# Kernel optimization log

Hardware: AMD Instinct MI355X
Metric: run time of the kernel (lower is better)

Reference implementation:

```python
import jax, jax.numpy as jnp
import numpy as np

D = 512        # d_model
DFF = 2048     # d_ffn
H = 8          # n_heads
L = 4          # n_blocks
EPS = 1e-5     # nn.LayerNorm default eps
NEG = -1e9


def _layer_norm(x, g, b):
    m = jnp.mean(x, axis=-1, keepdims=True)
    v = jnp.var(x, axis=-1, keepdims=True)
    return (x - m) / jnp.sqrt(v + EPS) * g + b


def setup_inputs() -> dict:
    key = jax.random.key(0)
    ks = jax.random.split(key, 6)
    B, S = 2, 2048
    s = 0.02
    x = jax.random.normal(ks[0], (B, S, D), dtype=jnp.float32)
    Wq = jax.random.normal(ks[1], (L, D, D), dtype=jnp.float32) * s
    Wk = jax.random.normal(ks[2], (L, D, D), dtype=jnp.float32) * s
    Wv = jax.random.normal(ks[3], (L, D, D), dtype=jnp.float32) * s
    W1 = jax.random.normal(ks[4], (L, D, DFF), dtype=jnp.float32) * s
    W2 = jax.random.normal(ks[5], (L, DFF, D), dtype=jnp.float32) * s
    z_d = jnp.zeros((L, D), dtype=jnp.float32)
    o_d = jnp.ones((L, D), dtype=jnp.float32)
    return {
        'x': x,
        'Wq': Wq, 'bq': z_d, 'Wk': Wk, 'bk': z_d, 'Wv': Wv, 'bv': z_d,
        'W1': W1, 'b1': jnp.zeros((L, DFF), dtype=jnp.float32),
        'W2': W2, 'b2': z_d,
        'g1': o_d, 'beta1': z_d, 'g2': o_d, 'beta2': z_d,
    }


def reference(x, Wq, bq, Wk, bk, Wv, bv, W1, b1, W2, b2, g1, beta1, g2, beta2):
    B, S, Dm = x.shape
    dk = Dm // H
    scale = 1.0 / (dk ** 0.5)

    def block(h, p):
        wq, bq_, wk, bk_, wv, bv_, w1, b1_, w2, b2_, g1_, be1, g2_, be2 = p
        # QKV projections, split heads: [B,S,D] -> [B,H,S,dk]
        q = (h @ wq + bq_).reshape(B, S, H, dk).transpose(0, 2, 1, 3)
        k = (h @ wk + bk_).reshape(B, S, H, dk).transpose(0, 2, 1, 3)
        v = (h @ wv + bv_).reshape(B, S, H, dk).transpose(0, 2, 1, 3)
        scores = jnp.einsum('bhqd,bhkd->bhqk', q, k) * scale
        # original quirk: padding=0, scores exactly equal to 0 get masked to -1e9
        scores = jnp.where(scores != 0, scores, NEG)
        probs = jax.nn.softmax(scores, axis=-1)
        attn = jnp.einsum('bhqk,bhkd->bhqd', probs, v)
        attn = attn.transpose(0, 2, 1, 3).reshape(B, S, Dm)
        h = _layer_norm(attn + h, g1_, be1)           # add_and_norm1
        ff = jax.nn.relu(h @ w1 + b1_) @ w2 + b2_     # position-wise FFN
        h = _layer_norm(h + ff, g2_, be2)             # add_and_norm2
        return h, None

    params = (Wq, bq, Wk, bk, Wv, bv, W1, b1, W2, b2, g1, beta1, g2, beta2)
    out, _ = jax.lax.scan(block, x, params)
    return out
```

## Files before the change

### kernel.cpp

```cpp
#include <hip/hip_runtime.h>
#include <stdint.h>
#include <math.h>


typedef __bf16 bf16_t;
typedef bf16_t bf16x8 __attribute__((ext_vector_type(8)));
typedef bf16_t bf16x4v __attribute__((ext_vector_type(4)));
typedef float  f32x4  __attribute__((ext_vector_type(4)));

__device__ __forceinline__ f32x4 mfma16(bf16x8 a, bf16x8 b, f32x4 c) {
    return __builtin_amdgcn_mfma_f32_16x16x32_bf16(a, b, c, 0, 0, 0);
}

__device__ __forceinline__ void cp16(const void* g, const void* l) {
    auto gp = reinterpret_cast<const __attribute__((address_space(1))) char*>(
        reinterpret_cast<uintptr_t>(g));
    auto lp = reinterpret_cast<__attribute__((address_space(3))) char*>(
        static_cast<uint32_t>(reinterpret_cast<uintptr_t>(l)));
    __builtin_amdgcn_global_load_lds((const __attribute__((address_space(1))) void*)gp,
                                     (__attribute__((address_space(3))) void*)lp,
                                     16, 0, 0);
}

__global__ void wconv_kernel(const float* __restrict__ Wq, const float* __restrict__ Wk,
                             const float* __restrict__ Wv, const float* __restrict__ W1,
                             const float* __restrict__ W2,
                             bf16_t* __restrict__ oQKV, bf16_t* __restrict__ oW1,
                             bf16_t* __restrict__ oW2)
{
    const int l = blockIdx.y;
    int t = blockIdx.x;
    const float* in; bf16_t* out; int Kd, Nd, tt;
    if (t < 192) {
        int m = t / 64; tt = t % 64; Kd = 512; Nd = 512;
        in  = (m == 0 ? Wq : m == 1 ? Wk : Wv) + (size_t)l * 512 * 512;
        out = oQKV + (size_t)l * 1536 * 512 + (size_t)m * 512 * 512;
    } else if (t < 448) {
        tt = t - 192; Kd = 512; Nd = 2048;
        in  = W1 + (size_t)l * 512 * 2048;
        out = oW1 + (size_t)l * 2048 * 512;
    } else {
        tt = t - 448; Kd = 2048; Nd = 512;
        in  = W2 + (size_t)l * 2048 * 512;
        out = oW2 + (size_t)l * 512 * 2048;
    }
    const int ntx = Nd >> 6;
    const int bk = (tt / ntx) * 64, bn = (tt % ntx) * 64;
    __shared__ float tile[64][65];
    const int tid = threadIdx.x;
    #pragma unroll
    for (int i = 0; i < 16; ++i) {
        int idx = i * 256 + tid; int r = idx >> 6, c = idx & 63;
        tile[r][c] = in[(size_t)(bk + r) * Nd + bn + c];
    }
    __syncthreads();
    #pragma unroll
    for (int i = 0; i < 4; ++i) {
        int idx = i * 256 + tid; int n = idx >> 4, kc = (idx & 15) * 4;
        bf16x4v o;
        o[0] = (bf16_t)tile[kc + 0][n];
        o[1] = (bf16_t)tile[kc + 1][n];
        o[2] = (bf16_t)tile[kc + 2][n];
        o[3] = (bf16_t)tile[kc + 3][n];
        *(bf16x4v*)&out[(size_t)(bn + n) * Kd + bk + kc] = o;
    }
}

__global__ void f2b_kernel(const float* __restrict__ in, bf16_t* __restrict__ out, int n)
{
    int i = (blockIdx.x * 256 + threadIdx.x) * 8;
    if (i >= n) return;
    float4 a = *(const float4*)(in + i);
    float4 b = *(const float4*)(in + i + 4);
    bf16x8 o;
    o[0] = (bf16_t)a.x; o[1] = (bf16_t)a.y; o[2] = (bf16_t)a.z; o[3] = (bf16_t)a.w;
    o[4] = (bf16_t)b.x; o[5] = (bf16_t)b.y; o[6] = (bf16_t)b.z; o[7] = (bf16_t)b.w;
    *(bf16x8*)(out + i) = o;
}

template<int MODE, bool RELU>
__global__ __launch_bounds__(256, 4) void gemm_kernel(
    const bf16_t* __restrict__ A, const bf16_t* __restrict__ Wt,
    const float* __restrict__ b0, const float* __restrict__ b1, const float* __restrict__ b2,
    void* __restrict__ o0, void* __restrict__ o1, void* __restrict__ o2,
    int N, int lda, int klen)
{
    __shared__ __align__(16) bf16_t lA[2][128 * 32];
    __shared__ __align__(16) bf16_t lB[2][128 * 32];
    const int tid = threadIdx.x;
    const int lane = tid & 63, w = tid >> 6;
    const int wm = w >> 1, wn = w & 1;
    const int l15 = lane & 15, quad = lane >> 4;
    const int row0 = blockIdx.y * 128, col0 = blockIdx.x * 128;
    const int kst = blockIdx.z * klen, kend = kst + klen;
    const int wbase = (tid & 192) * 16;

    f32x4 acc[4][4] = {};
    const char* Ab = (const char*)A;
    const char* Bb = (const char*)Wt;

    auto stage = [&](int k0, int buf) {
        #pragma unroll
        for (int p = 0; p < 2; ++p) {
            int o = (p * 256 + tid) * 16;
            int r = o >> 6, cb = o & 63;
            cp16(Ab + ((size_t)(row0 + r) * lda + k0) * 2 + cb, (char*)lA[buf] + p * 4096 + wbase);
            cp16(Bb + ((size_t)(col0 + r) * lda + k0) * 2 + cb, (char*)lB[buf] + p * 4096 + wbase);
        }
    };

    stage(kst, 0);
    int it = 0;
    for (int k0 = kst; k0 < kend; k0 += 32, ++it) {
        __syncthreads();
        if (k0 + 32 < kend) stage(k0 + 32, (it + 1) & 1);
        const bf16_t* cA = lA[it & 1];
        const bf16_t* cB = lB[it & 1];
        bf16x8 af[4], bv_[4];
        #pragma unroll
        for (int i = 0; i < 4; ++i)
            af[i] = *(const bf16x8*)&cA[(wm * 64 + i * 16 + l15) * 32 + quad * 8];
        #pragma unroll
        for (int i = 0; i < 4; ++i)
            bv_[i] = *(const bf16x8*)&cB[(wn * 64 + i * 16 + l15) * 32 + quad * 8];
        #pragma unroll
        for (int mi = 0; mi < 4; ++mi)
            #pragma unroll
            for (int ni = 0; ni < 4; ++ni)
                acc[mi][ni] = mfma16(af[mi], bv_[ni], acc[mi][ni]);
    }

    #pragma unroll
    for (int mi = 0; mi < 4; ++mi) {
        const int rowb = row0 + wm * 64 + mi * 16 + quad * 4;
        #pragma unroll
        for (int ni = 0; ni < 4; ++ni) {
            const int col = col0 + wn * 64 + ni * 16 + l15;
            if (MODE == 1) {
                const float bias = b0[col];
                #pragma unroll
                for (int r = 0; r < 4; ++r) {
                    float v = acc[mi][ni][r] + bias;
                    if (RELU) v = fmaxf(v, 0.f);
                    ((bf16_t*)o0)[(size_t)(rowb + r) * N + col] = (bf16_t)v;
                }
            } else if (MODE == 3) {
                bf16_t* op = (bf16_t*)o0 + (size_t)blockIdx.z * 4096 * 512;
                #pragma unroll
                for (int r = 0; r < 4; ++r)
                    op[(size_t)(rowb + r) * N + col] = (bf16_t)acc[mi][ni][r];
            } else {
                if (col < 512) {
                    const float bias = b0[col];
                    #pragma unroll
                    for (int r = 0; r < 4; ++r)
                        ((bf16_t*)o0)[(size_t)(rowb + r) * 512 + col] =
                            (bf16_t)((acc[mi][ni][r] + bias) * 0.18033688f);
                } else if (col < 1024) {
                    const int c = col - 512;
                    const float bias = b1[c];
                    #pragma unroll
                    for (int r = 0; r < 4; ++r)
                        ((bf16_t*)o1)[(size_t)(rowb + r) * 512 + c] =
                            (bf16_t)(acc[mi][ni][r] + bias);
                } else {
                    const int cv = col - 1024;
                    const int hh = cv >> 6, d = cv & 63;
                    const float bias = b2[cv];
                    const int b_ = rowb >> 11, s = rowb & 2047;
                    bf16x4v pk;
                    #pragma unroll
                    for (int r = 0; r < 4; ++r)
                        pk[r] = (bf16_t)(acc[mi][ni][r] + bias);
                    *(bf16x4v*)&((bf16_t*)o2)[(size_t)((b_ * 8 + hh) * 64 + d) * 2048 + s] = pk;
                }
            }
        }
    }
}

__global__ __launch_bounds__(256, 4) void attn_kernel(
    const bf16_t* __restrict__ Q, const bf16_t* __restrict__ Kg,
    const bf16_t* __restrict__ Vt, bf16_t* __restrict__ Op,
    float* __restrict__ Lb)
{
    __shared__ __align__(16) bf16_t lK[2][64 * 32];
    __shared__ __align__(16) bf16_t lV[2][64 * 32];
    __shared__ __align__(16) bf16_t lP[4][1152];
    const int tid = threadIdx.x;
    const int lane = tid & 63, w = tid >> 6;
    const int l15 = lane & 15, quad = lane >> 4;
    const int bh = blockIdx.x & 15, sp = blockIdx.x >> 4;
    const int b = bh >> 3, h = bh & 7;
    const int q0 = blockIdx.y * 128;
    const int kbase = sp * 512;
    const int wbase = w * 1024;
    const int srow = tid >> 2, scb = (tid & 3) * 16;

    bf16x8 qf[2][2];
    #pragma unroll
    for (int mi = 0; mi < 2; ++mi)
        #pragma unroll
        for (int ks = 0; ks < 2; ++ks)
            qf[mi][ks] = *(const bf16x8*)&Q[(size_t)(b * 2048 + q0 + w * 32 + mi * 16 + l15) * 512
                                            + h * 64 + ks * 32 + quad * 8];

    f32x4 oaccT[2][4] = {};
    float tsum[2][4] = {};

    for (int t = 0; t < 8; ++t) {
        const int k0 = kbase + t * 64;
        __syncthreads();
        #pragma unroll
        for (int ks = 0; ks < 2; ++ks)
            cp16((const char*)Kg + ((size_t)(b * 2048 + k0 + srow) * 512 + h * 64 + ks * 32) * 2 + scb,
                 (char*)lK[ks] + wbase);
        #pragma unroll
        for (int g = 0; g < 2; ++g)
            cp16((const char*)Vt + ((size_t)(bh * 64 + srow) * 2048 + k0 + g * 32) * 2 + scb,
                 (char*)lV[g] + wbase);
        __syncthreads();

        f32x4 sacc[2][4] = {};
        #pragma unroll
        for (int ni = 0; ni < 4; ++ni) {
            bf16x8 kf0 = *(const bf16x8*)&lK[0][(ni * 16 + l15) * 32 + quad * 8];
            bf16x8 kf1 = *(const bf16x8*)&lK[1][(ni * 16 + l15) * 32 + quad * 8];
            sacc[0][ni] = mfma16(qf[0][0], kf0, sacc[0][ni]);
            sacc[0][ni] = mfma16(qf[0][1], kf1, sacc[0][ni]);
            sacc[1][ni] = mfma16(qf[1][0], kf0, sacc[1][ni]);
            sacc[1][ni] = mfma16(qf[1][1], kf1, sacc[1][ni]);
        }

        #pragma unroll
        for (int mi = 0; mi < 2; ++mi)
            #pragma unroll
            for (int ni = 0; ni < 4; ++ni)
                #pragma unroll
                for (int r = 0; r < 4; ++r) {
                    float s = sacc[mi][ni][r];
                    float p_ = (s == 0.f) ? 0.f : __builtin_amdgcn_exp2f(s);
                    sacc[mi][ni][r] = p_;
                    tsum[mi][r] += p_;
                }

        #pragma unroll
        for (int kc = 0; kc < 2; ++kc) {
            #pragma unroll
            for (int mi = 0; mi < 2; ++mi)
                #pragma unroll
                for (int nn = 0; nn < 2; ++nn) {
                    const int ni = kc * 2 + nn;
                    #pragma unroll
                    for (int r = 0; r < 4; ++r)
                        lP[w][(mi * 16 + quad * 4 + r) * 36 + nn * 16 + l15] =
                            (bf16_t)sacc[mi][ni][r];
                }
            bf16x8 pf[2];
            #pragma unroll
            for (int mi = 0; mi < 2; ++mi) {
                bf16x4v p0 = *(const bf16x4v*)&lP[w][(mi * 16 + l15) * 36 + quad * 8];
                bf16x4v p1 = *(const bf16x4v*)&lP[w][(mi * 16 + l15) * 36 + quad * 8 + 4];
                #pragma unroll
                for (int j = 0; j < 4; ++j) { pf[mi][j] = p0[j]; pf[mi][4 + j] = p1[j]; }
            }
            #pragma unroll
            for (int nd = 0; nd < 4; ++nd) {
                bf16x8 vf = *(const bf16x8*)&lV[kc][(nd * 16 + l15) * 32 + quad * 8];
                oaccT[0][nd] = mfma16(vf, pf[0], oaccT[0][nd]);
                oaccT[1][nd] = mfma16(vf, pf[1], oaccT[1][nd]);
            }
        }
    }

    #pragma unroll
    for (int mi = 0; mi < 2; ++mi)
        #pragma unroll
        for (int r = 0; r < 4; ++r) {
            float s_ = tsum[mi][r];
            s_ += __shfl_xor(s_, 1);
            s_ += __shfl_xor(s_, 2);
            s_ += __shfl_xor(s_, 4);
            s_ += __shfl_xor(s_, 8);
            tsum[mi][r] = s_;
        }

    bf16_t* op = Op + (size_t)sp * 4096 * 512;
    #pragma unroll
    for (int mi = 0; mi < 2; ++mi) {
        const int row = b * 2048 + q0 + w * 32 + mi * 16 + l15;
        #pragma unroll
        for (int nd = 0; nd < 4; ++nd) {
            bf16x4v pk;
            #pragma unroll
            for (int r = 0; r < 4; ++r) pk[r] = (bf16_t)oaccT[mi][nd][r];
            *(bf16x4v*)&op[(size_t)row * 512 + h * 64 + nd * 16 + quad * 4] = pk;
        }
        if (l15 == 0) {
            #pragma unroll
            for (int r = 0; r < 4; ++r) {
                int rr = b * 2048 + q0 + w * 32 + mi * 16 + quad * 4 + r;
                Lb[((size_t)rr * 8 + h) * 4 + sp] = tsum[mi][r];
            }
        }
    }
}

__global__ void lnadd_c(const bf16_t* __restrict__ Op, const float* __restrict__ Lb,
                        const float* __restrict__ hin,
                        const float* __restrict__ g, const float* __restrict__ be,
                        float* __restrict__ Yf, bf16_t* __restrict__ Yb)
{
    const int row = blockIdx.x * 4 + (threadIdx.x >> 6);
    const int lane = threadIdx.x & 63;
    const int c0 = lane * 8;
    const int head = lane >> 3;
    const float4 l4 = *(const float4*)&Lb[((size_t)row * 8 + head) * 4];
    const float linv = 1.f / (l4.x + l4.y + l4.z + l4.w);
    const size_t idx = (size_t)row * 512 + c0;
    bf16x8 o0 = *(const bf16x8*)&Op[idx];
    bf16x8 o1 = *(const bf16x8*)&Op[idx + 2097152];
    bf16x8 o2 = *(const bf16x8*)&Op[idx + 2 * 2097152];
    bf16x8 o3 = *(const bf16x8*)&Op[idx + 3 * 2097152];
    float4 h0 = *(const float4*)&hin[idx];
    float4 h1 = *(const float4*)&hin[idx + 4];
    const float hr[8] = {h0.x, h0.y, h0.z, h0.w, h1.x, h1.y, h1.z, h1.w};
    float v[8]; float s = 0.f;
    #pragma unroll
    for (int j = 0; j < 8; ++j) {
        v[j] = ((float)o0[j] + (float)o1[j] + (float)o2[j] + (float)o3[j]) * linv + hr[j];
        s += v[j];
    }
    #pragma unroll
    for (int off = 32; off >= 1; off >>= 1) s += __shfl_xor(s, off);
    const float mean = s * (1.f / 512.f);
    float vs = 0.f;
    #pragma unroll
    for (int j = 0; j < 8; ++j) { float d = v[j] - mean; vs += d * d; }
    #pragma unroll
    for (int off = 32; off >= 1; off >>= 1) vs += __shfl_xor(vs, off);
    const float inv = rsqrtf(vs * (1.f / 512.f) + 1e-5f);
    float4 g0 = *(const float4*)&g[c0], g1 = *(const float4*)&g[c0 + 4];
    float4 b0 = *(const float4*)&be[c0], b1 = *(const float4*)&be[c0 + 4];
    const float gg[8] = {g0.x, g0.y, g0.z, g0.w, g1.x, g1.y, g1.z, g1.w};
    const float bb[8] = {b0.x, b0.y, b0.z, b0.w, b1.x, b1.y, b1.z, b1.w};
    float y[8]; bf16x8 yb;
    #pragma unroll
    for (int j = 0; j < 8; ++j) {
        y[j] = (v[j] - mean) * inv * gg[j] + bb[j];
        yb[j] = (bf16_t)y[j];
    }
    *(float4*)&Yf[idx]     = make_float4(y[0], y[1], y[2], y[3]);
    *(float4*)&Yf[idx + 4] = make_float4(y[4], y[5], y[6], y[7]);
    *(bf16x8*)&Yb[idx] = yb;
}

__global__ void lnadd_f(const bf16_t* __restrict__ G, const float* __restrict__ bias,
                        const float* __restrict__ hres, const float* __restrict__ g,
                        const float* __restrict__ be,
                        float* __restrict__ Yf, bf16_t* __restrict__ Yb)
{
    const int row = blockIdx.x * 4 + (threadIdx.x >> 6);
    const int lane = threadIdx.x & 63;
    const int c0 = lane * 8;
    const size_t idx = (size_t)row * 512 + c0;
    bf16x8 o0 = *(const bf16x8*)&G[idx];
    bf16x8 o1 = *(const bf16x8*)&G[idx + 2097152];
    bf16x8 o2 = *(const bf16x8*)&G[idx + 2 * 2097152];
    bf16x8 o3 = *(const bf16x8*)&G[idx + 3 * 2097152];
    float4 h0 = *(const float4*)&hres[idx];
    float4 h1 = *(const float4*)&hres[idx + 4];
    float4 bi0 = *(const float4*)&bias[c0], bi1 = *(const float4*)&bias[c0 + 4];
    const float hr[8] = {h0.x, h0.y, h0.z, h0.w, h1.x, h1.y, h1.z, h1.w};
    const float bs[8] = {bi0.x, bi0.y, bi0.z, bi0.w, bi1.x, bi1.y, bi1.z, bi1.w};
    float v[8]; float s = 0.f;
    #pragma unroll
    for (int j = 0; j < 8; ++j) {
        v[j] = (float)o0[j] + (float)o1[j] + (float)o2[j] + (float)o3[j] + bs[j] + hr[j];
        s += v[j];
    }
    #pragma unroll
    for (int off = 32; off >= 1; off >>= 1) s += __shfl_xor(s, off);
    const float mean = s * (1.f / 512.f);
    float vs = 0.f;
    #pragma unroll
    for (int j = 0; j < 8; ++j) { float d = v[j] - mean; vs += d * d; }
    #pragma unroll
    for (int off = 32; off >= 1; off >>= 1) vs += __shfl_xor(vs, off);
    const float inv = rsqrtf(vs * (1.f / 512.f) + 1e-5f);
    float4 g0 = *(const float4*)&g[c0], g1 = *(const float4*)&g[c0 + 4];
    float4 b0 = *(const float4*)&be[c0], b1 = *(const float4*)&be[c0 + 4];
    const float gg[8] = {g0.x, g0.y, g0.z, g0.w, g1.x, g1.y, g1.z, g1.w};
    const float bb[8] = {b0.x, b0.y, b0.z, b0.w, b1.x, b1.y, b1.z, b1.w};
    float y[8]; bf16x8 yb;
    #pragma unroll
    for (int j = 0; j < 8; ++j) {
        y[j] = (v[j] - mean) * inv * gg[j] + bb[j];
        yb[j] = (bf16_t)y[j];
    }
    *(float4*)&Yf[idx]     = make_float4(y[0], y[1], y[2], y[3]);
    *(float4*)&Yf[idx + 4] = make_float4(y[4], y[5], y[6], y[7]);
    *(bf16x8*)&Yb[idx] = yb;
}

extern "C" void kernel_launch(void* const* d_in, const int* in_sizes, int n_in,
                              void* d_out, int out_size, void* d_ws, size_t ws_size,
                              hipStream_t stream)
{
    const float* x   = (const float*)d_in[0];
    const float* Wq  = (const float*)d_in[1];
    const float* bq  = (const float*)d_in[2];
    const float* Wk  = (const float*)d_in[3];
    const float* bk  = (const float*)d_in[4];
    const float* Wv  = (const float*)d_in[5];
    const float* bv  = (const float*)d_in[6];
    const float* W1  = (const float*)d_in[7];
    const float* b1  = (const float*)d_in[8];
    const float* W2  = (const float*)d_in[9];
    const float* b2  = (const float*)d_in[10];
    const float* g1  = (const float*)d_in[11];
    const float* be1 = (const float*)d_in[12];
    const float* g2  = (const float*)d_in[13];
    const float* be2 = (const float*)d_in[14];

    char* p = (char*)d_ws;
    auto carve = [&](size_t bytes) { char* r = p; p += (bytes + 255) & ~(size_t)255; return r; };
    bf16_t* wQKV = (bf16_t*)carve(4UL * 1536 * 512 * 2);
    bf16_t* wW1t = (bf16_t*)carve(4UL * 2048 * 512 * 2);
    bf16_t* wW2t = (bf16_t*)carve(4UL * 512 * 2048 * 2);
    bf16_t* hbf  = (bf16_t*)carve(4096UL * 512 * 2);
    bf16_t* h2b  = (bf16_t*)carve(4096UL * 512 * 2);
    bf16_t* Fb   = (bf16_t*)carve(4096UL * 2048 * 2);
    bf16_t* R2   = (bf16_t*)carve(4UL * 4096 * 512 * 2);
    float*  Lbuf = (float*)carve(4096UL * 8 * 4 * 4);
    float*  h2f  = (float*)carve(4096UL * 512 * 4);
    float*  hf   = (float*)carve(4096UL * 512 * 4);
    bf16_t* Qb  = Fb;
    bf16_t* Kb  = Fb + 4096UL * 512;
    bf16_t* Vtb = Fb + 2UL * 4096 * 512;

    wconv_kernel<<<dim3(704, 4), 256, 0, stream>>>(Wq, Wk, Wv, W1, W2, wQKV, wW1t, wW2t);
    f2b_kernel<<<dim3(1024), 256, 0, stream>>>(x, hbf, 4096 * 512);

    const float* hin = x;
    for (int l = 0; l < 4; ++l) {
        gemm_kernel<2, false><<<dim3(12, 32, 1), 256, 0, stream>>>(
            hbf, wQKV + (size_t)l * 1536 * 512,
            bq + l * 512, bk + l * 512, bv + l * 512,
            Qb, Kb, Vtb, 1536, 512, 512);
        attn_kernel<<<dim3(64, 16), 256, 0, stream>>>(Qb, Kb, Vtb, R2, Lbuf);
        lnadd_c<<<dim3(1024), 256, 0, stream>>>(R2, Lbuf, hin,
                                                g1 + l * 512, be1 + l * 512, h2f, h2b);
        gemm_kernel<1, true><<<dim3(16, 32, 1), 256, 0, stream>>>(
            h2b, wW1t + (size_t)l * 2048 * 512,
            b1 + l * 2048, nullptr, nullptr,
            Fb, nullptr, nullptr, 2048, 512, 512);
        gemm_kernel<3, false><<<dim3(4, 32, 4), 256, 0, stream>>>(
            Fb, wW2t + (size_t)l * 512 * 2048,
            nullptr, nullptr, nullptr,
            R2, nullptr, nullptr, 512, 2048, 512);
        float* yout = (l == 3) ? (float*)d_out : hf;
        lnadd_f<<<dim3(1024), 256, 0, stream>>>(R2, b2 + l * 512, h2f,
                                                g2 + l * 512, be2 + l * 512, yout, hbf);
        hin = hf;
    }
    (void)in_sizes; (void)n_in; (void)out_size; (void)ws_size;
}
```

Measured before the change: 506.6 us.

## Halve GEMM M-tile to 64 rows and double attention query tile to 256

The GEMM kernel gets a TM template parameter and all three GEMMs now run with 64-row M tiles, doubling the grid to give more blocks for the 256 CUs at the cost of less reuse of each B tile. The attention kernel now covers 256 query rows per block (64 per wave), so each staged K/V tile feeds twice as many MFMAs and K/V loads are amortised. In exchange it needs more registers, its launch bounds drop to 2 blocks per SM, and the attention grid is halved, which may leave CUs underused.

```diff
diff --git a/kernel.cpp b/kernel.cpp
--- a/kernel.cpp
+++ b/kernel.cpp
@@ -78,33 +78,39 @@
     *(bf16x8*)(out + i) = o;
 }
 
-template<int MODE, bool RELU>
+template<int MODE, bool RELU, int TM>
 __global__ __launch_bounds__(256, 4) void gemm_kernel(
     const bf16_t* __restrict__ A, const bf16_t* __restrict__ Wt,
     const float* __restrict__ b0, const float* __restrict__ b1, const float* __restrict__ b2,
     void* __restrict__ o0, void* __restrict__ o1, void* __restrict__ o2,
     int N, int lda, int klen)
 {
-    __shared__ __align__(16) bf16_t lA[2][128 * 32];
+    constexpr int MI = TM / 32;
+    __shared__ __align__(16) bf16_t lA[2][TM * 32];
     __shared__ __align__(16) bf16_t lB[2][128 * 32];
     const int tid = threadIdx.x;
     const int lane = tid & 63, w = tid >> 6;
     const int wm = w >> 1, wn = w & 1;
     const int l15 = lane & 15, quad = lane >> 4;
-    const int row0 = blockIdx.y * 128, col0 = blockIdx.x * 128;
+    const int row0 = blockIdx.y * TM, col0 = blockIdx.x * 128;
     const int kst = blockIdx.z * klen, kend = kst + klen;
     const int wbase = (tid & 192) * 16;
 
-    f32x4 acc[4][4] = {};
+    f32x4 acc[MI][4] = {};
     const char* Ab = (const char*)A;
     const char* Bb = (const char*)Wt;
 
     auto stage = [&](int k0, int buf) {
+        #pragma unroll
+        for (int p = 0; p < TM / 64; ++p) {
+            int o = (p * 256 + tid) * 16;
+            int r = o >> 6, cb = o & 63;
+            cp16(Ab + ((size_t)(row0 + r) * lda + k0) * 2 + cb, (char*)lA[buf] + p * 4096 + wbase);
+        }
         #pragma unroll
         for (int p = 0; p < 2; ++p) {
             int o = (p * 256 + tid) * 16;
             int r = o >> 6, cb = o & 63;
-            cp16(Ab + ((size_t)(row0 + r) * lda + k0) * 2 + cb, (char*)lA[buf] + p * 4096 + wbase);
             cp16(Bb + ((size_t)(col0 + r) * lda + k0) * 2 + cb, (char*)lB[buf] + p * 4096 + wbase);
         }
     };
@@ -116,23 +122,23 @@
         if (k0 + 32 < kend) stage(k0 + 32, (it + 1) & 1);
         const bf16_t* cA = lA[it & 1];
         const bf16_t* cB = lB[it & 1];
-        bf16x8 af[4], bv_[4];
-        #pragma unroll
-        for (int i = 0; i < 4; ++i)
-            af[i] = *(const bf16x8*)&cA[(wm * 64 + i * 16 + l15) * 32 + quad * 8];
+        bf16x8 af[MI], bv_[4];
+        #pragma unroll
+        for (int i = 0; i < MI; ++i)
+            af[i] = *(const bf16x8*)&cA[(wm * (TM / 2) + i * 16 + l15) * 32 + quad * 8];
         #pragma unroll
         for (int i = 0; i < 4; ++i)
             bv_[i] = *(const bf16x8*)&cB[(wn * 64 + i * 16 + l15) * 32 + quad * 8];
         #pragma unroll
-        for (int mi = 0; mi < 4; ++mi)
+        for (int mi = 0; mi < MI; ++mi)
             #pragma unroll
             for (int ni = 0; ni < 4; ++ni)
                 acc[mi][ni] = mfma16(af[mi], bv_[ni], acc[mi][ni]);
     }
 
     #pragma unroll
-    for (int mi = 0; mi < 4; ++mi) {
-        const int rowb = row0 + wm * 64 + mi * 16 + quad * 4;
+    for (int mi = 0; mi < MI; ++mi) {
+        const int rowb = row0 + wm * (TM / 2) + mi * 16 + quad * 4;
         #pragma unroll
         for (int ni = 0; ni < 4; ++ni) {
             const int col = col0 + wn * 64 + ni * 16 + l15;
@@ -179,34 +185,34 @@
     }
 }
 
-__global__ __launch_bounds__(256, 4) void attn_kernel(
+__global__ __launch_bounds__(256, 2) void attn_kernel(
     const bf16_t* __restrict__ Q, const bf16_t* __restrict__ Kg,
     const bf16_t* __restrict__ Vt, bf16_t* __restrict__ Op,
     float* __restrict__ Lb)
 {
     __shared__ __align__(16) bf16_t lK[2][64 * 32];
     __shared__ __align__(16) bf16_t lV[2][64 * 32];
-    __shared__ __align__(16) bf16_t lP[4][1152];
+    __shared__ __align__(16) bf16_t lP[4][64 * 36];
     const int tid = threadIdx.x;
     const int lane = tid & 63, w = tid >> 6;
     const int l15 = lane & 15, quad = lane >> 4;
     const int bh = blockIdx.x & 15, sp = blockIdx.x >> 4;
     const int b = bh >> 3, h = bh & 7;
-    const int q0 = blockIdx.y * 128;
+    const int q0 = blockIdx.y * 256;
     const int kbase = sp * 512;
     const int wbase = w * 1024;
     const int srow = tid >> 2, scb = (tid & 3) * 16;
 
-    bf16x8 qf[2][2];
-    #pragma unroll
-    for (int mi = 0; mi < 2; ++mi)
+    bf16x8 qf[4][2];
+    #pragma unroll
+    for (int mi = 0; mi < 4; ++mi)
         #pragma unroll
         for (int ks = 0; ks < 2; ++ks)
-            qf[mi][ks] = *(const bf16x8*)&Q[(size_t)(b * 2048 + q0 + w * 32 + mi * 16 + l15) * 512
+            qf[mi][ks] = *(const bf16x8*)&Q[(size_t)(b * 2048 + q0 + w * 64 + mi * 16 + l15) * 512
                                             + h * 64 + ks * 32 + quad * 8];
 
-    f32x4 oaccT[2][4] = {};
-    float tsum[2][4] = {};
+    f32x4 oaccT[4][4] = {};
+    float tsum[4][4] = {};
 
     for (int t = 0; t < 8; ++t) {
         const int k0 = kbase + t * 64;
@@ -221,19 +227,20 @@
                  (char*)lV[g] + wbase);
         __syncthreads();
 
-        f32x4 sacc[2][4] = {};
+        f32x4 sacc[4][4] = {};
         #pragma unroll
         for (int ni = 0; ni < 4; ++ni) {
             bf16x8 kf0 = *(const bf16x8*)&lK[0][(ni * 16 + l15) * 32 + quad * 8];
             bf16x8 kf1 = *(const bf16x8*)&lK[1][(ni * 16 + l15) * 32 + quad * 8];
-            sacc[0][ni] = mfma16(qf[0][0], kf0, sacc[0][ni]);
-            sacc[0][ni] = mfma16(qf[0][1], kf1, sacc[0][ni]);
-            sacc[1][ni] = mfma16(qf[1][0], kf0, sacc[1][ni]);
-            sacc[1][ni] = mfma16(qf[1][1], kf1, sacc[1][ni]);
-        }
-
-        #pragma unroll
-        for (int mi = 0; mi < 2; ++mi)
+            #pragma unroll
+            for (int mi = 0; mi < 4; ++mi) {
+                sacc[mi][ni] = mfma16(qf[mi][0], kf0, sacc[mi][ni]);
+                sacc[mi][ni] = mfma16(qf[mi][1], kf1, sacc[mi][ni]);
+            }
+        }
+
+        #pragma unroll
+        for (int mi = 0; mi < 4; ++mi)
             #pragma unroll
             for (int ni = 0; ni < 4; ++ni)
                 #pragma unroll
@@ -247,7 +254,7 @@
         #pragma unroll
         for (int kc = 0; kc < 2; ++kc) {
             #pragma unroll
-            for (int mi = 0; mi < 2; ++mi)
+            for (int mi = 0; mi < 4; ++mi)
                 #pragma unroll
                 for (int nn = 0; nn < 2; ++nn) {
                     const int ni = kc * 2 + nn;
@@ -256,9 +263,9 @@
                         lP[w][(mi * 16 + quad * 4 + r) * 36 + nn * 16 + l15] =
                             (bf16_t)sacc[mi][ni][r];
                 }
-            bf16x8 pf[2];
-            #pragma unroll
-            for (int mi = 0; mi < 2; ++mi) {
+            bf16x8 pf[4];
+            #pragma unroll
+            for (int mi = 0; mi < 4; ++mi) {
                 bf16x4v p0 = *(const bf16x4v*)&lP[w][(mi * 16 + l15) * 36 + quad * 8];
                 bf16x4v p1 = *(const bf16x4v*)&lP[w][(mi * 16 + l15) * 36 + quad * 8 + 4];
                 #pragma unroll
@@ -267,14 +274,15 @@
             #pragma unroll
             for (int nd = 0; nd < 4; ++nd) {
                 bf16x8 vf = *(const bf16x8*)&lV[kc][(nd * 16 + l15) * 32 + quad * 8];
-                oaccT[0][nd] = mfma16(vf, pf[0], oaccT[0][nd]);
-                oaccT[1][nd] = mfma16(vf, pf[1], oaccT[1][nd]);
+                #pragma unroll
+                for (int mi = 0; mi < 4; ++mi)
+                    oaccT[mi][nd] = mfma16(vf, pf[mi], oaccT[mi][nd]);
             }
         }
     }
 
     #pragma unroll
-    for (int mi = 0; mi < 2; ++mi)
+    for (int mi = 0; mi < 4; ++mi)
         #pragma unroll
         for (int r = 0; r < 4; ++r) {
             float s_ = tsum[mi][r];
@@ -287,8 +295,8 @@
 
     bf16_t* op = Op + (size_t)sp * 4096 * 512;
     #pragma unroll
-    for (int mi = 0; mi < 2; ++mi) {
-        const int row = b * 2048 + q0 + w * 32 + mi * 16 + l15;
+    for (int mi = 0; mi < 4; ++mi) {
+        const int row = b * 2048 + q0 + w * 64 + mi * 16 + l15;
         #pragma unroll
         for (int nd = 0; nd < 4; ++nd) {
             bf16x4v pk;
@@ -299,7 +307,7 @@
         if (l15 == 0) {
             #pragma unroll
             for (int r = 0; r < 4; ++r) {
-                int rr = b * 2048 + q0 + w * 32 + mi * 16 + quad * 4 + r;
+                int rr = b * 2048 + q0 + w * 64 + mi * 16 + quad * 4 + r;
                 Lb[((size_t)rr * 8 + h) * 4 + sp] = tsum[mi][r];
             }
         }
@@ -444,18 +452,18 @@
 
     const float* hin = x;
     for (int l = 0; l < 4; ++l) {
-        gemm_kernel<2, false><<<dim3(12, 32, 1), 256, 0, stream>>>(
+        gemm_kernel<2, false, 64><<<dim3(12, 64, 1), 256, 0, stream>>>(
             hbf, wQKV + (size_t)l * 1536 * 512,
             bq + l * 512, bk + l * 512, bv + l * 512,
             Qb, Kb, Vtb, 1536, 512, 512);
-        attn_kernel<<<dim3(64, 16), 256, 0, stream>>>(Qb, Kb, Vtb, R2, Lbuf);
+        attn_kernel<<<dim3(64, 8), 256, 0, stream>>>(Qb, Kb, Vtb, R2, Lbuf);
         lnadd_c<<<dim3(1024), 256, 0, stream>>>(R2, Lbuf, hin,
                                                 g1 + l * 512, be1 + l * 512, h2f, h2b);
-        gemm_kernel<1, true><<<dim3(16, 32, 1), 256, 0, stream>>>(
+        gemm_kernel<1, true, 64><<<dim3(16, 64, 1), 256, 0, stream>>>(
             h2b, wW1t + (size_t)l * 2048 * 512,
             b1 + l * 2048, nullptr, nullptr,
             Fb, nullptr, nullptr, 2048, 512, 512);
-        gemm_kernel<3, false><<<dim3(4, 32, 4), 256, 0, stream>>>(
+        gemm_kernel<3, false, 64><<<dim3(4, 64, 4), 256, 0, stream>>>(
             Fb, wW2t + (size_t)l * 512 * 2048,
             nullptr, nullptr, nullptr,
             R2, nullptr, nullptr, 512, 2048, 512);
```

Result: slower. 524.6 us (+3.5%).

## Load GEMM weight fragments directly from global into registers, bypassing LDS

Applied to the files above, without the earlier changes.

The B (weight) operand is no longer staged through shared memory. Each lane now loads its MFMA fragments straight from global memory into registers, with a register double buffer (bcur/bnext) to prefetch the next k-slice. This halves LDS usage and removes the LDS reads for B, which may raise occupancy. In exchange, the two wave columns that share the same B columns now fetch them redundantly. The per-lane 16-byte global loads are strided by lda, so they coalesce poorly, and global latency is exposed inside the k-loop.

```diff
diff --git a/kernel.cpp b/kernel.cpp
--- a/kernel.cpp
+++ b/kernel.cpp
@@ -86,7 +86,6 @@
     int N, int lda, int klen)
 {
     __shared__ __align__(16) bf16_t lA[2][128 * 32];
-    __shared__ __align__(16) bf16_t lB[2][128 * 32];
     const int tid = threadIdx.x;
     const int lane = tid & 63, w = tid >> 6;
     const int wm = w >> 1, wn = w & 1;
@@ -97,37 +96,51 @@
 
     f32x4 acc[4][4] = {};
     const char* Ab = (const char*)A;
-    const char* Bb = (const char*)Wt;
-
-    auto stage = [&](int k0, int buf) {
+
+    const bf16_t* Bp[4];
+    #pragma unroll
+    for (int ni = 0; ni < 4; ++ni)
+        Bp[ni] = Wt + (size_t)(col0 + wn * 64 + ni * 16 + l15) * lda + quad * 8;
+
+    auto stageA = [&](int k0, int buf) {
         #pragma unroll
         for (int p = 0; p < 2; ++p) {
             int o = (p * 256 + tid) * 16;
             int r = o >> 6, cb = o & 63;
             cp16(Ab + ((size_t)(row0 + r) * lda + k0) * 2 + cb, (char*)lA[buf] + p * 4096 + wbase);
-            cp16(Bb + ((size_t)(col0 + r) * lda + k0) * 2 + cb, (char*)lB[buf] + p * 4096 + wbase);
         }
     };
 
-    stage(kst, 0);
+    stageA(kst, 0);
+    bf16x8 bcur[4], bnext[4];
+    #pragma unroll
+    for (int ni = 0; ni < 4; ++ni)
+        bcur[ni] = *(const bf16x8*)(Bp[ni] + kst);
+
     int it = 0;
     for (int k0 = kst; k0 < kend; k0 += 32, ++it) {
+        const bool more = (k0 + 32 < kend);
         __syncthreads();
-        if (k0 + 32 < kend) stage(k0 + 32, (it + 1) & 1);
+        if (more) {
+            stageA(k0 + 32, (it + 1) & 1);
+            #pragma unroll
+            for (int ni = 0; ni < 4; ++ni)
+                bnext[ni] = *(const bf16x8*)(Bp[ni] + k0 + 32);
+        }
         const bf16_t* cA = lA[it & 1];
-        const bf16_t* cB = lB[it & 1];
-        bf16x8 af[4], bv_[4];
+        bf16x8 af[4];
         #pragma unroll
         for (int i = 0; i < 4; ++i)
             af[i] = *(const bf16x8*)&cA[(wm * 64 + i * 16 + l15) * 32 + quad * 8];
         #pragma unroll
-        for (int i = 0; i < 4; ++i)
-            bv_[i] = *(const bf16x8*)&cB[(wn * 64 + i * 16 + l15) * 32 + quad * 8];
-        #pragma unroll
         for (int mi = 0; mi < 4; ++mi)
             #pragma unroll
             for (int ni = 0; ni < 4; ++ni)
-                acc[mi][ni] = mfma16(af[mi], bv_[ni], acc[mi][ni]);
+                acc[mi][ni] = mfma16(af[mi], bcur[ni], acc[mi][ni]);
+        if (more) {
+            #pragma unroll
+            for (int ni = 0; ni < 4; ++ni) bcur[ni] = bnext[ni];
+        }
     }
 
     #pragma unroll
```

Result: slower. 594.8 us (+17.4%).

## Fuse layernorm epilogues into attention and FFN2 kernels via last-block counters

Applied to the files above, without the earlier changes.

Removes the separate lnadd_c and lnadd_f kernels. The last-arriving block for each row tile, detected through an atomic counter plus threadfence, now does the split-reduction sum, residual add and layernorm. The x-to-bf16 conversion is also folded into the weight-conversion launch, and a memset resets the counters. This saves launches and global round-trips, but the final block does a serial 128-row epilogue that can form a tail.

```diff
diff --git a/kernel.cpp b/kernel.cpp
--- a/kernel.cpp
+++ b/kernel.cpp
@@ -24,12 +24,24 @@
 
 __global__ void wconv_kernel(const float* __restrict__ Wq, const float* __restrict__ Wk,
                              const float* __restrict__ Wv, const float* __restrict__ W1,
-                             const float* __restrict__ W2,
+                             const float* __restrict__ W2, const float* __restrict__ x,
                              bf16_t* __restrict__ oQKV, bf16_t* __restrict__ oW1,
-                             bf16_t* __restrict__ oW2)
+                             bf16_t* __restrict__ oW2, bf16_t* __restrict__ xb)
 {
     const int l = blockIdx.y;
     int t = blockIdx.x;
+    const int tid = threadIdx.x;
+    if (t >= 704) {
+        const int chunk = (t - 704) + 256 * l;
+        const int i = chunk * 2048 + tid * 8;
+        float4 a = *(const float4*)(x + i);
+        float4 b = *(const float4*)(x + i + 4);
+        bf16x8 o;
+        o[0] = (bf16_t)a.x; o[1] = (bf16_t)a.y; o[2] = (bf16_t)a.z; o[3] = (bf16_t)a.w;
+        o[4] = (bf16_t)b.x; o[5] = (bf16_t)b.y; o[6] = (bf16_t)b.z; o[7] = (bf16_t)b.w;
+        *(bf16x8*)(xb + i) = o;
+        return;
+    }
     const float* in; bf16_t* out; int Kd, Nd, tt;
     if (t < 192) {
         int m = t / 64; tt = t % 64; Kd = 512; Nd = 512;
@@ -47,7 +59,6 @@
     const int ntx = Nd >> 6;
     const int bk = (tt / ntx) * 64, bn = (tt % ntx) * 64;
     __shared__ float tile[64][65];
-    const int tid = threadIdx.x;
     #pragma unroll
     for (int i = 0; i < 16; ++i) {
         int idx = i * 256 + tid; int r = idx >> 6, c = idx & 63;
@@ -66,16 +77,36 @@
     }
 }
 
-__global__ void f2b_kernel(const float* __restrict__ in, bf16_t* __restrict__ out, int n)
+__device__ __forceinline__ void ln_row(const float v[8], const float* __restrict__ g,
+                                       const float* __restrict__ be, int c0,
+                                       float* __restrict__ Yf, bf16_t* __restrict__ Yb,
+                                       size_t idx)
 {
-    int i = (blockIdx.x * 256 + threadIdx.x) * 8;
-    if (i >= n) return;
-    float4 a = *(const float4*)(in + i);
-    float4 b = *(const float4*)(in + i + 4);
-    bf16x8 o;
-    o[0] = (bf16_t)a.x; o[1] = (bf16_t)a.y; o[2] = (bf16_t)a.z; o[3] = (bf16_t)a.w;
-    o[4] = (bf16_t)b.x; o[5] = (bf16_t)b.y; o[6] = (bf16_t)b.z; o[7] = (bf16_t)b.w;
-    *(bf16x8*)(out + i) = o;
+    float s = 0.f;
+    #pragma unroll
+    for (int j = 0; j < 8; ++j) s += v[j];
+    #pragma unroll
+    for (int off = 32; off >= 1; off >>= 1) s += __shfl_xor(s, off);
+    const float mean = s * (1.f / 512.f);
+    float vs = 0.f;
+    #pragma unroll
+    for (int j = 0; j < 8; ++j) { float d = v[j] - mean; vs += d * d; }
+    #pragma unroll
+    for (int off = 32; off >= 1; off >>= 1) vs += __shfl_xor(vs, off);
+    const float inv = rsqrtf(vs * (1.f / 512.f) + 1e-5f);
+    float4 g0 = *(const float4*)&g[c0], g1 = *(const float4*)&g[c0 + 4];
+    float4 b0 = *(const float4*)&be[c0], b1 = *(const float4*)&be[c0 + 4];
+    const float gg[8] = {g0.x, g0.y, g0.z, g0.w, g1.x, g1.y, g1.z, g1.w};
+    const float bb[8] = {b0.x, b0.y, b0.z, b0.w, b1.x, b1.y, b1.z, b1.w};
+    float y[8]; bf16x8 yb;
+    #pragma unroll
+    for (int j = 0; j < 8; ++j) {
+        y[j] = (v[j] - mean) * inv * gg[j] + bb[j];
+        yb[j] = (bf16_t)y[j];
+    }
+    *(float4*)&Yf[idx]     = make_float4(y[0], y[1], y[2], y[3]);
+    *(float4*)&Yf[idx + 4] = make_float4(y[4], y[5], y[6], y[7]);
+    *(bf16x8*)&Yb[idx] = yb;
 }
 
 template<int MODE, bool RELU>
@@ -83,7 +114,10 @@
     const bf16_t* __restrict__ A, const bf16_t* __restrict__ Wt,
     const float* __restrict__ b0, const float* __restrict__ b1, const float* __restrict__ b2,
     void* __restrict__ o0, void* __restrict__ o1, void* __restrict__ o2,
-    int N, int lda, int klen)
+    int N, int lda, int klen,
+    const float* __restrict__ hres, const float* __restrict__ lng,
+    const float* __restrict__ lnbe, float* __restrict__ Yf, bf16_t* __restrict__ Yb,
+    unsigned* __restrict__ ctr)
 {
     __shared__ __align__(16) bf16_t lA[2][128 * 32];
     __shared__ __align__(16) bf16_t lB[2][128 * 32];
@@ -177,12 +211,48 @@
             }
         }
     }
+
+    if (MODE == 3) {
+        __threadfence();
+        __syncthreads();
+        __shared__ int lastF;
+        if (tid == 0) lastF = (atomicAdd(&ctr[blockIdx.y], 1u) == 15u) ? 1 : 0;
+        __syncthreads();
+        if (lastF) {
+            __threadfence();
+            const bf16_t* G = (const bf16_t*)o0;
+            const int lane2 = tid & 63, wv = tid >> 6;
+            const int c0 = lane2 * 8;
+            float4 bi0 = *(const float4*)&b0[c0], bi1 = *(const float4*)&b0[c0 + 4];
+            const float bs[8] = {bi0.x, bi0.y, bi0.z, bi0.w, bi1.x, bi1.y, bi1.z, bi1.w};
+            for (int rr = wv; rr < 128; rr += 4) {
+                const int row = row0 + rr;
+                const size_t idx = (size_t)row * 512 + c0;
+                bf16x8 p0 = *(const bf16x8*)&G[idx];
+                bf16x8 p1 = *(const bf16x8*)&G[idx + 2097152];
+                bf16x8 p2 = *(const bf16x8*)&G[idx + 2 * 2097152];
+                bf16x8 p3 = *(const bf16x8*)&G[idx + 3 * 2097152];
+                float4 h0 = *(const float4*)&hres[idx];
+                float4 h1 = *(const float4*)&hres[idx + 4];
+                const float hr[8] = {h0.x, h0.y, h0.z, h0.w, h1.x, h1.y, h1.z, h1.w};
+                float v[8];
+                #pragma unroll
+                for (int j = 0; j < 8; ++j)
+                    v[j] = (float)p0[j] + (float)p1[j] + (float)p2[j] + (float)p3[j]
+                         + bs[j] + hr[j];
+                ln_row(v, lng, lnbe, c0, Yf, Yb, idx);
+            }
+        }
+    }
 }
 
 __global__ __launch_bounds__(256, 4) void attn_kernel(
     const bf16_t* __restrict__ Q, const bf16_t* __restrict__ Kg,
     const bf16_t* __restrict__ Vt, bf16_t* __restrict__ Op,
-    float* __restrict__ Lb)
+    float* __restrict__ Lb,
+    const float* __restrict__ hin, const float* __restrict__ lng,
+    const float* __restrict__ lnbe, float* __restrict__ Yf,
+    bf16_t* __restrict__ Yb, unsigned* __restrict__ ctr)
 {
     __shared__ __align__(16) bf16_t lK[2][64 * 32];
     __shared__ __align__(16) bf16_t lV[2][64 * 32];
@@ -304,103 +374,38 @@
             }
         }
     }
-}
-
-__global__ void lnadd_c(const bf16_t* __restrict__ Op, const float* __restrict__ Lb,
-                        const float* __restrict__ hin,
-                        const float* __restrict__ g, const float* __restrict__ be,
-                        float* __restrict__ Yf, bf16_t* __restrict__ Yb)
-{
-    const int row = blockIdx.x * 4 + (threadIdx.x >> 6);
-    const int lane = threadIdx.x & 63;
-    const int c0 = lane * 8;
-    const int head = lane >> 3;
-    const float4 l4 = *(const float4*)&Lb[((size_t)row * 8 + head) * 4];
-    const float linv = 1.f / (l4.x + l4.y + l4.z + l4.w);
-    const size_t idx = (size_t)row * 512 + c0;
-    bf16x8 o0 = *(const bf16x8*)&Op[idx];
-    bf16x8 o1 = *(const bf16x8*)&Op[idx + 2097152];
-    bf16x8 o2 = *(const bf16x8*)&Op[idx + 2 * 2097152];
-    bf16x8 o3 = *(const bf16x8*)&Op[idx + 3 * 2097152];
-    float4 h0 = *(const float4*)&hin[idx];
-    float4 h1 = *(const float4*)&hin[idx + 4];
-    const float hr[8] = {h0.x, h0.y, h0.z, h0.w, h1.x, h1.y, h1.z, h1.w};
-    float v[8]; float s = 0.f;
-    #pragma unroll
-    for (int j = 0; j < 8; ++j) {
-        v[j] = ((float)o0[j] + (float)o1[j] + (float)o2[j] + (float)o3[j]) * linv + hr[j];
-        s += v[j];
-    }
-    #pragma unroll
-    for (int off = 32; off >= 1; off >>= 1) s += __shfl_xor(s, off);
-    const float mean = s * (1.f / 512.f);
-    float vs = 0.f;
-    #pragma unroll
-    for (int j = 0; j < 8; ++j) { float d = v[j] - mean; vs += d * d; }
-    #pragma unroll
-    for (int off = 32; off >= 1; off >>= 1) vs += __shfl_xor(vs, off);
-    const float inv = rsqrtf(vs * (1.f / 512.f) + 1e-5f);
-    float4 g0 = *(const float4*)&g[c0], g1 = *(const float4*)&g[c0 + 4];
-    float4 b0 = *(const float4*)&be[c0], b1 = *(const float4*)&be[c0 + 4];
-    const float gg[8] = {g0.x, g0.y, g0.z, g0.w, g1.x, g1.y, g1.z, g1.w};
-    const float bb[8] = {b0.x, b0.y, b0.z, b0.w, b1.x, b1.y, b1.z, b1.w};
-    float y[8]; bf16x8 yb;
-    #pragma unroll
-    for (int j = 0; j < 8; ++j) {
-        y[j] = (v[j] - mean) * inv * gg[j] + bb[j];
-        yb[j] = (bf16_t)y[j];
-    }
-    *(float4*)&Yf[idx]     = make_float4(y[0], y[1], y[2], y[3]);
-    *(float4*)&Yf[idx + 4] = make_float4(y[4], y[5], y[6], y[7]);
-    *(bf16x8*)&Yb[idx] = yb;
-}
-
-__global__ void lnadd_f(const bf16_t* __restrict__ G, const float* __restrict__ bias,
-                        const float* __restrict__ hres, const float* __restrict__ g,
-                        const float* __restrict__ be,
-                        float* __restrict__ Yf, bf16_t* __restrict__ Yb)
-{
-    const int row = blockIdx.x * 4 + (threadIdx.x >> 6);
-    const int lane = threadIdx.x & 63;
-    const int c0 = lane * 8;
-    const size_t idx = (size_t)row * 512 + c0;
-    bf16x8 o0 = *(const bf16x8*)&G[idx];
-    bf16x8 o1 = *(const bf16x8*)&G[idx + 2097152];
-    bf16x8 o2 = *(const bf16x8*)&G[idx + 2 * 2097152];
-    bf16x8 o3 = *(const bf16x8*)&G[idx + 3 * 2097152];
-    float4 h0 = *(const float4*)&hres[idx];
-    float4 h1 = *(const float4*)&hres[idx + 4];
-    float4 bi0 = *(const float4*)&bias[c0], bi1 = *(const float4*)&bias[c0 + 4];
-    const float hr[8] = {h0.x, h0.y, h0.z, h0.w, h1.x, h1.y, h1.z, h1.w};
-    const float bs[8] = {bi0.x, bi0.y, bi0.z, bi0.w, bi1.x, bi1.y, bi1.z, bi1.w};
-    float v[8]; float s = 0.f;
-    #pragma unroll
-    for (int j = 0; j < 8; ++j) {
-        v[j] = (float)o0[j] + (float)o1[j] + (float)o2[j] + (float)o3[j] + bs[j] + hr[j];
-        s += v[j];
-    }
-    #pragma unroll
-    for (int off = 32; off >= 1; off >>= 1) s += __shfl_xor(s, off);
-    const float mean = s * (1.f / 512.f);
-    float vs = 0.f;
-    #pragma unroll
-    for (int j = 0; j < 8; ++j) { float d = v[j] - mean; vs += d * d; }
-    #pragma unroll
-    for (int off = 32; off >= 1; off >>= 1) vs += __shfl_xor(vs, off);
-    const float inv = rsqrtf(vs * (1.f / 512.f) + 1e-5f);
-    float4 g0 = *(const float4*)&g[c0], g1 = *(const float4*)&g[c0 + 4];
-    float4 b0 = *(const float4*)&be[c0], b1 = *(const float4*)&be[c0 + 4];
-    const float gg[8] = {g0.x, g0.y, g0.z, g0.w, g1.x, g1.y, g1.z, g1.w};
-    const float bb[8] = {b0.x, b0.y, b0.z, b0.w, b1.x, b1.y, b1.z, b1.w};
-    float y[8]; bf16x8 yb;
-    #pragma unroll
-    for (int j = 0; j < 8; ++j) {
-        y[j] = (v[j] - mean) * inv * gg[j] + bb[j];
-        yb[j] = (bf16_t)y[j];
-    }
-    *(float4*)&Yf[idx]     = make_float4(y[0], y[1], y[2], y[3]);
-    *(float4*)&Yf[idx + 4] = make_float4(y[4], y[5], y[6], y[7]);
-    *(bf16x8*)&Yb[idx] = yb;
+
+    __threadfence();
+    __syncthreads();
+    __shared__ int lastA;
+    if (tid == 0) lastA = (atomicAdd(&ctr[b * 16 + blockIdx.y], 1u) == 31u) ? 1 : 0;
+    __syncthreads();
+    if (lastA) {
+        __threadfence();
+        const int lane2 = tid & 63, wv = tid >> 6;
+        const int c0 = lane2 * 8;
+        const int head2 = lane2 >> 3;
+        const int rowbase = b * 2048 + q0;
+        for (int rr = wv; rr < 128; rr += 4) {
+            const int row = rowbase + rr;
+            const float4 l4 = *(const float4*)&Lb[((size_t)row * 8 + head2) * 4];
+            const float linv = 1.f / (l4.x + l4.y + l4.z + l4.w);
+            const size_t idx = (size_t)row * 512 + c0;
+            bf16x8 p0 = *(const bf16x8*)&Op[idx];
+            bf16x8 p1 = *(const bf16x8*)&Op[idx + 2097152];
+            bf16x8 p2 = *(const bf16x8*)&Op[idx + 2 * 2097152];
+            bf16x8 p3 = *(const bf16x8*)&Op[idx + 3 * 2097152];
+            float4 h0 = *(const float4*)&hin[idx];
+            float4 h1 = *(const float4*)&hin[idx + 4];
+            const float hr[8] = {h0.x, h0.y, h0.z, h0.w, h1.x, h1.y, h1.z, h1.w};
+            float v[8];
+            #pragma unroll
+            for (int j = 0; j < 8; ++j)
+                v[j] = ((float)p0[j] + (float)p1[j] + (float)p2[j] + (float)p3[j]) * linv
+                     + hr[j];
+            ln_row(v, lng, lnbe, c0, Yf, Yb, idx);
+        }
+    }
 }
 
 extern "C" void kernel_launch(void* const* d_in, const int* in_sizes, int n_in,
@@ -435,33 +440,38 @@
     float*  Lbuf = (float*)carve(4096UL * 8 * 4 * 4);
     float*  h2f  = (float*)carve(4096UL * 512 * 4);
     float*  hf   = (float*)carve(4096UL * 512 * 4);
+    unsigned* ctr = (unsigned*)carve(4UL * 64 * 4);
     bf16_t* Qb  = Fb;
     bf16_t* Kb  = Fb + 4096UL * 512;
     bf16_t* Vtb = Fb + 2UL * 4096 * 512;
 
-    wconv_kernel<<<dim3(704, 4), 256, 0, stream>>>(Wq, Wk, Wv, W1, W2, wQKV, wW1t, wW2t);
-    f2b_kernel<<<dim3(1024), 256, 0, stream>>>(x, hbf, 4096 * 512);
+    hipMemsetAsync(ctr, 0, 4UL * 64 * 4, stream);
+    wconv_kernel<<<dim3(960, 4), 256, 0, stream>>>(Wq, Wk, Wv, W1, W2, x,
+                                                   wQKV, wW1t, wW2t, hbf);
 
     const float* hin = x;
     for (int l = 0; l < 4; ++l) {
+        unsigned* ctrA = ctr + l * 64;
+        unsigned* ctrF = ctr + l * 64 + 32;
         gemm_kernel<2, false><<<dim3(12, 32, 1), 256, 0, stream>>>(
             hbf, wQKV + (size_t)l * 1536 * 512,
             bq + l * 512, bk + l * 512, bv + l * 512,
-            Qb, Kb, Vtb, 1536, 512, 512);
-        attn_kernel<<<dim3(64, 16), 256, 0, stream>>>(Qb, Kb, Vtb, R2, Lbuf);
-        lnadd_c<<<dim3(1024), 256, 0, stream>>>(R2, Lbuf, hin,
-                                                g1 + l * 512, be1 + l * 512, h2f, h2b);
+            Qb, Kb, Vtb, 1536, 512, 512,
+            nullptr, nullptr, nullptr, nullptr, nullptr, nullptr);
+        attn_kernel<<<dim3(64, 16), 256, 0, stream>>>(
+            Qb, Kb, Vtb, R2, Lbuf,
+            hin, g1 + l * 512, be1 + l * 512, h2f, h2b, ctrA);
         gemm_kernel<1, true><<<dim3(16, 32, 1), 256, 0, stream>>>(
             h2b, wW1t + (size_t)l * 2048 * 512,
             b1 + l * 2048, nullptr, nullptr,
-            Fb, nullptr, nullptr, 2048, 512, 512);
+            Fb, nullptr, nullptr, 2048, 512, 512,
+            nullptr, nullptr, nullptr, nullptr, nullptr, nullptr);
+        float* yout = (l == 3) ? (float*)d_out : hf;
         gemm_kernel<3, false><<<dim3(4, 32, 4), 256, 0, stream>>>(
             Fb, wW2t + (size_t)l * 512 * 2048,
-            nullptr, nullptr, nullptr,
-            R2, nullptr, nullptr, 512, 2048, 512);
-        float* yout = (l == 3) ? (float*)d_out : hf;
-        lnadd_f<<<dim3(1024), 256, 0, stream>>>(R2, b2 + l * 512, h2f,
-                                                g2 + l * 512, be2 + l * 512, yout, hbf);
+            b2 + l * 512, nullptr, nullptr,
+            R2, nullptr, nullptr, 512, 2048, 512,
+            h2f, g2 + l * 512, be2 + l * 512, yout, hbf, ctrF);
         hin = hf;
     }
     (void)in_sizes; (void)n_in; (void)out_size; (void)ws_size;
```

After: 1.724 ms. 240% more time.
